# Kernel optimization log

Hardware: AMD Instinct MI355X
Metric: run time of the kernel (lower is better)

## Reference

```python
import jax, jax.numpy as jnp
import numpy as np

TEMPERATURE = 0.025

def _l2norm(x, eps=1e-12):
    # torch F.normalize(p=2, dim=-1): x / max(||x||, eps)
    n = jnp.sqrt(jnp.sum(x * x, axis=-1, keepdims=True))
    return x / jnp.maximum(n, eps)

def setup_inputs() -> dict:
    key = jax.random.key(0)
    ks = jax.random.split(key, 8)
    B, C, S = 512, 640, 14
    T = S * S  # 196
    H = T // 6  # 32
    sc1 = 1.0 / np.sqrt(T)
    sc2 = 1.0 / np.sqrt(H)
    return {
        "class_feat": jax.random.normal(ks[0], (B, C, S, S), jnp.float32),
        "query_feat": jax.random.normal(ks[1], (B, C, S, S), jnp.float32),
        "cw1": jax.random.normal(ks[2], (T, H), jnp.float32) * sc1,
        "cb1": jnp.zeros((H,), jnp.float32),
        "cw2": jax.random.normal(ks[3], (H, T), jnp.float32) * sc2,
        "cb2": jnp.zeros((T,), jnp.float32),
        "qw1": jax.random.normal(ks[4], (T, H), jnp.float32) * sc1,
        "qb1": jnp.zeros((H,), jnp.float32),
        "qw2": jax.random.normal(ks[5], (H, T), jnp.float32) * sc2,
        "qb2": jnp.zeros((T,), jnp.float32),
    }

def _apply_attention(feat, corr, w1, b1, w2, b2):
    # corr: [B, T, T]; kernel MLP on mean over dim=1 -> [B, T]
    B, C, S, _ = feat.shape
    m = corr.mean(axis=1)                              # [B, T]
    kernel = jax.nn.relu(m @ w1 + b1) @ w2 + b2        # [B, T]
    logits = jnp.einsum('btu,bu->bt', corr, kernel) / TEMPERATURE
    attn = jax.nn.softmax(logits, axis=1)              # softmax over tokens
    return feat * (1.0 + attn.reshape(B, 1, S, S))

def reference(class_feat, query_feat, cw1, cb1, cw2, cb2, qw1, qb1, qw2, qb2):
    B, C, S, _ = class_feat.shape
    T = S * S
    # tokens: [B, T, C], L2-normalized over channels
    ct = _l2norm(class_feat.reshape(B, C, T).transpose(0, 2, 1))
    qt = _l2norm(query_feat.reshape(B, C, T).transpose(0, 2, 1))
    corr = jnp.einsum('btc,buc->btu', ct, qt)          # [B, T, T]
    class_w = _apply_attention(class_feat, corr, cw1, cb1, cw2, cb2)
    query_w = _apply_attention(query_feat, corr.transpose(0, 2, 1), qw1, qb1, qw2, qb2)
    return (class_w, query_w)
```

## Files before the change

kernel.cpp:

```cpp
#include <hip/hip_runtime.h>

constexpr int kB = 512;
constexpr int kC = 640;
constexpr int kT = 196;
constexpr int kTP = 224;
constexpr int kH = 32;
constexpr int kKSTEP = 32;

typedef __bf16 bf16x8 __attribute__((ext_vector_type(8)));
typedef float  f32x16 __attribute__((ext_vector_type(16)));

__device__ __forceinline__ unsigned f2bfbits(float x) {
  unsigned u = __builtin_bit_cast(unsigned, x);
  return (u + 0x7FFFu + ((u >> 16) & 1u)) >> 16;
}
__device__ __forceinline__ float bf2f(unsigned short v) {
  return __builtin_bit_cast(float, (unsigned)v << 16);
}

__global__ __launch_bounds__(448) void corr_kernel(
    const float* __restrict__ cf, const float* __restrict__ qf,
    unsigned short* __restrict__ corr_out)
{
  __shared__ int Al[(kKSTEP/2) * kTP];
  __shared__ int Bl[(kKSTEP/2) * kTP];
  __shared__ float ssA[kTP], ssB[kTP], invA[kTP], invB[kTP];

  const int b    = blockIdx.x;
  const int tid  = threadIdx.x;
  const int wave = tid >> 6;
  const int lane = tid & 63;
  const int hf   = lane >> 5;
  const int l31  = lane & 31;

  const float4* Ap = (const float4*)(cf + (size_t)b * kC * kT);
  const float4* Bp = (const float4*)(qf + (size_t)b * kC * kT);

  const int t4 = tid % 56;
  const int kr = tid / 56;
  const bool realcol = (t4 < 49);

  if (tid < kTP) { ssA[tid] = 0.f; ssB[tid] = 0.f; }

  float4 sa = {0.f,0.f,0.f,0.f}, sb = {0.f,0.f,0.f,0.f};

  f32x16 acc[7];
#pragma unroll
  for (int c = 0; c < 7; ++c)
#pragma unroll
    for (int r = 0; r < 16; ++r) acc[c][r] = 0.f;

  const int mrow = 32 * wave + l31;

  for (int s = 0; s < kC / kKSTEP; ++s) {
    const int k0 = s * kKSTEP;
    __syncthreads();
#pragma unroll
    for (int i = 0; i < 2; ++i) {
      const int k2 = kr + 8 * i;
      float4 a0 = {0,0,0,0}, a1 = {0,0,0,0}, b0 = {0,0,0,0}, b1 = {0,0,0,0};
      if (realcol) {
        const size_t r0 = (size_t)(k0 + 2 * k2) * 49 + t4;
        a0 = Ap[r0]; a1 = Ap[r0 + 49];
        b0 = Bp[r0]; b1 = Bp[r0 + 49];
      }
      sa.x += a0.x*a0.x + a1.x*a1.x;  sa.y += a0.y*a0.y + a1.y*a1.y;
      sa.z += a0.z*a0.z + a1.z*a1.z;  sa.w += a0.w*a0.w + a1.w*a1.w;
      sb.x += b0.x*b0.x + b1.x*b1.x;  sb.y += b0.y*b0.y + b1.y*b1.y;
      sb.z += b0.z*b0.z + b1.z*b1.z;  sb.w += b0.w*b0.w + b1.w*b1.w;
      uint4 aw, bw;
      aw.x = f2bfbits(a0.x) | (f2bfbits(a1.x) << 16);
      aw.y = f2bfbits(a0.y) | (f2bfbits(a1.y) << 16);
      aw.z = f2bfbits(a0.z) | (f2bfbits(a1.z) << 16);
      aw.w = f2bfbits(a0.w) | (f2bfbits(a1.w) << 16);
      bw.x = f2bfbits(b0.x) | (f2bfbits(b1.x) << 16);
      bw.y = f2bfbits(b0.y) | (f2bfbits(b1.y) << 16);
      bw.z = f2bfbits(b0.z) | (f2bfbits(b1.z) << 16);
      bw.w = f2bfbits(b0.w) | (f2bfbits(b1.w) << 16);
      ((uint4*)Al)[k2 * 56 + t4] = aw;
      ((uint4*)Bl)[k2 * 56 + t4] = bw;
    }
    __syncthreads();
#pragma unroll
    for (int kk = 0; kk < 2; ++kk) {
      const int base = (kk * 8 + hf * 4) * kTP;
      int4 av;
      av.x = Al[base          + mrow];
      av.y = Al[base + kTP    + mrow];
      av.z = Al[base + 2*kTP  + mrow];
      av.w = Al[base + 3*kTP  + mrow];
      bf16x8 af = __builtin_bit_cast(bf16x8, av);
#pragma unroll
      for (int c = 0; c < 7; ++c) {
        const int nrow = 32 * c + l31;
        int4 bv;
        bv.x = Bl[base          + nrow];
        bv.y = Bl[base + kTP    + nrow];
        bv.z = Bl[base + 2*kTP  + nrow];
        bv.w = Bl[base + 3*kTP  + nrow];
        bf16x8 bfv = __builtin_bit_cast(bf16x8, bv);
        acc[c] = __builtin_amdgcn_mfma_f32_32x32x16_bf16(af, bfv, acc[c], 0, 0, 0);
      }
    }
  }

  if (realcol) {
    atomicAdd(&ssA[4*t4+0], sa.x); atomicAdd(&ssA[4*t4+1], sa.y);
    atomicAdd(&ssA[4*t4+2], sa.z); atomicAdd(&ssA[4*t4+3], sa.w);
    atomicAdd(&ssB[4*t4+0], sb.x); atomicAdd(&ssB[4*t4+1], sb.y);
    atomicAdd(&ssB[4*t4+2], sb.z); atomicAdd(&ssB[4*t4+3], sb.w);
  }
  __syncthreads();
  if (tid < kTP) {
    invA[tid] = 1.0f / fmaxf(sqrtf(ssA[tid]), 1e-12f);
    invB[tid] = 1.0f / fmaxf(sqrtf(ssB[tid]), 1e-12f);
  }
  __syncthreads();

  unsigned short* co = corr_out + (size_t)b * kT * kT;
#pragma unroll
  for (int c = 0; c < 7; ++c) {
    const int u = 32 * c + l31;
    if (u < kT) {
      const float ivu = invB[u];
#pragma unroll
      for (int r = 0; r < 16; ++r) {
        const int t = 32 * wave + (r & 3) + 8 * (r >> 2) + 4 * hf;
        if (t < kT) {
          co[t * kT + u] = (unsigned short)f2bfbits(acc[c][r] * invA[t] * ivu);
        }
      }
    }
  }
}

__device__ __forceinline__ void softmax196(float lgv, int tid, float* red, float* outp) {
  red[tid] = lgv;
  __syncthreads();
  for (int o = 128; o > 0; o >>= 1) {
    if (tid < o) red[tid] = fmaxf(red[tid], red[tid + o]);
    __syncthreads();
  }
  const float mx = red[0];
  __syncthreads();
  const float e = (tid < kT) ? __expf(lgv - mx) : 0.f;
  red[tid] = e;
  __syncthreads();
  for (int o = 128; o > 0; o >>= 1) {
    if (tid < o) red[tid] += red[tid + o];
    __syncthreads();
  }
  const float inv = 1.0f / red[0];
  if (tid < kT) outp[tid] = e * inv;
  __syncthreads();
}

__global__ __launch_bounds__(256) void attn_kernel(
    const unsigned short* __restrict__ corr,
    const float* __restrict__ w1c, const float* __restrict__ b1c,
    const float* __restrict__ w2c, const float* __restrict__ b2c,
    const float* __restrict__ w1q, const float* __restrict__ b1q,
    const float* __restrict__ w2q, const float* __restrict__ b2q,
    float* __restrict__ attnC, float* __restrict__ attnQ)
{
  __shared__ __align__(16) unsigned short cs[kT * kT];
  __shared__ float mC[kT], mQ[kT], hid[kH], kern[kT], red[256];

  const int b = blockIdx.x, tid = threadIdx.x;
  {
    const uint4* src = (const uint4*)(corr + (size_t)b * kT * kT);
    uint4* dst = (uint4*)cs;
    for (int i = tid; i < kT * kT / 8; i += 256) dst[i] = src[i];
  }
  __syncthreads();

  if (tid < kT) {
    float s = 0.f, s2 = 0.f;
    for (int t = 0; t < kT; ++t) s  += bf2f(cs[t * kT + tid]);
    for (int u = 0; u < kT; ++u) s2 += bf2f(cs[tid * kT + u]);
    mC[tid] = s  * (1.0f / kT);
    mQ[tid] = s2 * (1.0f / kT);
  }
  __syncthreads();

  if (tid < kH) {
    float s = b1c[tid];
    for (int u = 0; u < kT; ++u) s += mC[u] * w1c[u * kH + tid];
    hid[tid] = fmaxf(s, 0.f);
  }
  __syncthreads();
  if (tid < kT) {
    float s = b2c[tid];
    for (int h = 0; h < kH; ++h) s += hid[h] * w2c[h * kT + tid];
    kern[tid] = s;
  }
  __syncthreads();
  float lgv = -3.4e38f;
  if (tid < kT) {
    float s = 0.f;
    for (int u = 0; u < kT; ++u) s += bf2f(cs[tid * kT + u]) * kern[u];
    lgv = s * 40.0f;
  }
  softmax196(lgv, tid, red, attnC + (size_t)b * kT);

  if (tid < kH) {
    float s = b1q[tid];
    for (int u = 0; u < kT; ++u) s += mQ[u] * w1q[u * kH + tid];
    hid[tid] = fmaxf(s, 0.f);
  }
  __syncthreads();
  if (tid < kT) {
    float s = b2q[tid];
    for (int h = 0; h < kH; ++h) s += hid[h] * w2q[h * kT + tid];
    kern[tid] = s;
  }
  __syncthreads();
  lgv = -3.4e38f;
  if (tid < kT) {
    float s = 0.f;
    for (int t = 0; t < kT; ++t) s += bf2f(cs[t * kT + tid]) * kern[t];
    lgv = s * 40.0f;
  }
  softmax196(lgv, tid, red, attnQ + (size_t)b * kT);
}

__global__ __launch_bounds__(256) void scale_kernel(
    const float4* __restrict__ cf, const float4* __restrict__ qf,
    const float* __restrict__ attnC, const float* __restrict__ attnQ,
    float4* __restrict__ out)
{
  constexpr unsigned NC4 = (unsigned)kB * kC * 49u;
  const unsigned i = blockIdx.x * 256u + threadIdx.x;
  unsigned j;
  const float4* fp;
  const float* ap;
  if (i < NC4) { j = i;       fp = cf; ap = attnC; }
  else         { j = i - NC4; fp = qf; ap = attnQ; }
  const unsigned col = j % 49u;
  const unsigned bc  = j / 49u;
  const unsigned b   = bc / (unsigned)kC;
  const float4 f = fp[j];
  const float4 a = *(const float4*)(ap + (size_t)b * kT + col * 4u);
  float4 r;
  r.x = f.x * (1.f + a.x);
  r.y = f.y * (1.f + a.y);
  r.z = f.z * (1.f + a.z);
  r.w = f.w * (1.f + a.w);
  out[i] = r;
}

extern "C" void kernel_launch(void* const* d_in, const int* in_sizes, int n_in,
                              void* d_out, int out_size, void* d_ws, size_t ws_size,
                              hipStream_t stream) {
  const float* cf  = (const float*)d_in[0];
  const float* qf  = (const float*)d_in[1];
  const float* cw1 = (const float*)d_in[2];
  const float* cb1 = (const float*)d_in[3];
  const float* cw2 = (const float*)d_in[4];
  const float* cb2 = (const float*)d_in[5];
  const float* qw1 = (const float*)d_in[6];
  const float* qb1 = (const float*)d_in[7];
  const float* qw2 = (const float*)d_in[8];
  const float* qb2 = (const float*)d_in[9];
  float* out = (float*)d_out;

  char* ws = (char*)d_ws;
  unsigned short* corr = (unsigned short*)ws;
  float* attn_c = (float*)(ws + (size_t)kB * kT * kT * 2);
  float* attn_q = attn_c + (size_t)kB * kT;

  corr_kernel<<<kB, 448, 0, stream>>>(cf, qf, corr);
  attn_kernel<<<kB, 256, 0, stream>>>(corr, cw1, cb1, cw2, cb2,
                                      qw1, qb1, qw2, qb2, attn_c, attn_q);
  constexpr unsigned total4 = 2u * (unsigned)kB * kC * 49u;
  scale_kernel<<<total4 / 256u, 256, 0, stream>>>(
      (const float4*)cf, (const float4*)qf, attn_c, attn_q, (float4*)out);
}
```

Measured before the change: 963.7 us.

## Fuse correlation and attention kernels, computing MLP and logits from MFMA registers

Merges the correlation GEMM kernel with the attention kernel so the 196x196 correlation matrix stays in MFMA accumulator registers. Row and column means and both logit matvecs are computed there with shuffles and shared atomics, so the bf16 corr matrix is never written to or reread from global memory. The K loop is also double-buffered in LDS, with the next slice's global loads prefetched into registers so only one barrier is needed per step. This removes a kernel launch and the corr round trip, at the cost of more LDS and register pressure and an fp32 rather than bf16-rounded correlation.

```diff
diff --git a/kernel.cpp b/kernel.cpp
--- a/kernel.cpp
+++ b/kernel.cpp
@@ -6,6 +6,7 @@
 constexpr int kTP = 224;
 constexpr int kH = 32;
 constexpr int kKSTEP = 32;
+constexpr int kNS = kC / kKSTEP;
 
 typedef __bf16 bf16x8 __attribute__((ext_vector_type(8)));
 typedef float  f32x16 __attribute__((ext_vector_type(16)));
@@ -14,17 +15,23 @@
   unsigned u = __builtin_bit_cast(unsigned, x);
   return (u + 0x7FFFu + ((u >> 16) & 1u)) >> 16;
 }
-__device__ __forceinline__ float bf2f(unsigned short v) {
-  return __builtin_bit_cast(float, (unsigned)v << 16);
-}
-
-__global__ __launch_bounds__(448) void corr_kernel(
+
+__global__ __launch_bounds__(448) void fused_corr_attn(
     const float* __restrict__ cf, const float* __restrict__ qf,
-    unsigned short* __restrict__ corr_out)
+    const float* __restrict__ w1c, const float* __restrict__ b1c,
+    const float* __restrict__ w2c, const float* __restrict__ b2c,
+    const float* __restrict__ w1q, const float* __restrict__ b1q,
+    const float* __restrict__ w2q, const float* __restrict__ b2q,
+    float* __restrict__ attnC, float* __restrict__ attnQ)
 {
-  __shared__ int Al[(kKSTEP/2) * kTP];
-  __shared__ int Bl[(kKSTEP/2) * kTP];
+  __shared__ int Al[2][(kKSTEP/2) * kTP];
+  __shared__ int Bl[2][(kKSTEP/2) * kTP];
   __shared__ float ssA[kTP], ssB[kTP], invA[kTP], invB[kTP];
+  __shared__ float colsum[kTP], rowsum[kTP];
+  __shared__ float hidC[kH], hidQ[kH];
+  __shared__ float kernC[kTP], kernQ[kTP];
+  __shared__ float lgC[kTP], lgQ[kTP];
+  __shared__ float red[256];
 
   const int b    = blockIdx.x;
   const int tid  = threadIdx.x;
@@ -40,7 +47,12 @@
   const int kr = tid / 56;
   const bool realcol = (t4 < 49);
 
-  if (tid < kTP) { ssA[tid] = 0.f; ssB[tid] = 0.f; }
+  if (tid < kTP) {
+    ssA[tid] = 0.f; ssB[tid] = 0.f;
+    colsum[tid] = 0.f; lgQ[tid] = 0.f;
+  }
+  if (tid < kH)        hidC[tid] = 0.f;
+  else if (tid < 2*kH) hidQ[tid - kH] = 0.f;
 
   float4 sa = {0.f,0.f,0.f,0.f}, sb = {0.f,0.f,0.f,0.f};
 
@@ -52,18 +64,26 @@
 
   const int mrow = 32 * wave + l31;
 
-  for (int s = 0; s < kC / kKSTEP; ++s) {
-    const int k0 = s * kKSTEP;
-    __syncthreads();
+  float4 pa0[2], pa1[2], pb0[2], pb1[2];
+#pragma unroll
+  for (int i = 0; i < 2; ++i) {
+    pa0[i] = make_float4(0.f,0.f,0.f,0.f); pa1[i] = pa0[i];
+    pb0[i] = pa0[i];                        pb1[i] = pa0[i];
+    const int k2 = kr + 8 * i;
+    if (realcol) {
+      const size_t r0 = (size_t)(2 * k2) * 49 + t4;
+      pa0[i] = Ap[r0]; pa1[i] = Ap[r0 + 49];
+      pb0[i] = Bp[r0]; pb1[i] = Bp[r0 + 49];
+    }
+  }
+
+  for (int s = 0; s < kNS; ++s) {
+    uint4* Aw = (uint4*)Al[s & 1];
+    uint4* Bw = (uint4*)Bl[s & 1];
 #pragma unroll
     for (int i = 0; i < 2; ++i) {
       const int k2 = kr + 8 * i;
-      float4 a0 = {0,0,0,0}, a1 = {0,0,0,0}, b0 = {0,0,0,0}, b1 = {0,0,0,0};
-      if (realcol) {
-        const size_t r0 = (size_t)(k0 + 2 * k2) * 49 + t4;
-        a0 = Ap[r0]; a1 = Ap[r0 + 49];
-        b0 = Bp[r0]; b1 = Bp[r0 + 49];
-      }
+      const float4 a0 = pa0[i], a1 = pa1[i], b0 = pb0[i], b1 = pb1[i];
       sa.x += a0.x*a0.x + a1.x*a1.x;  sa.y += a0.y*a0.y + a1.y*a1.y;
       sa.z += a0.z*a0.z + a1.z*a1.z;  sa.w += a0.w*a0.w + a1.w*a1.w;
       sb.x += b0.x*b0.x + b1.x*b1.x;  sb.y += b0.y*b0.y + b1.y*b1.y;
@@ -77,27 +97,41 @@
       bw.y = f2bfbits(b0.y) | (f2bfbits(b1.y) << 16);
       bw.z = f2bfbits(b0.z) | (f2bfbits(b1.z) << 16);
       bw.w = f2bfbits(b0.w) | (f2bfbits(b1.w) << 16);
-      ((uint4*)Al)[k2 * 56 + t4] = aw;
-      ((uint4*)Bl)[k2 * 56 + t4] = bw;
-    }
-    __syncthreads();
+      Aw[k2 * 56 + t4] = aw;
+      Bw[k2 * 56 + t4] = bw;
+    }
+    if (s + 1 < kNS) {
+      const int k0n = (s + 1) * kKSTEP;
+#pragma unroll
+      for (int i = 0; i < 2; ++i) {
+        const int k2 = kr + 8 * i;
+        if (realcol) {
+          const size_t r0 = (size_t)(k0n + 2 * k2) * 49 + t4;
+          pa0[i] = Ap[r0]; pa1[i] = Ap[r0 + 49];
+          pb0[i] = Bp[r0]; pb1[i] = Bp[r0 + 49];
+        }
+      }
+    }
+    __syncthreads();
+    const int* Ar = Al[s & 1];
+    const int* Br = Bl[s & 1];
 #pragma unroll
     for (int kk = 0; kk < 2; ++kk) {
       const int base = (kk * 8 + hf * 4) * kTP;
       int4 av;
-      av.x = Al[base          + mrow];
-      av.y = Al[base + kTP    + mrow];
-      av.z = Al[base + 2*kTP  + mrow];
-      av.w = Al[base + 3*kTP  + mrow];
+      av.x = Ar[base          + mrow];
+      av.y = Ar[base + kTP    + mrow];
+      av.z = Ar[base + 2*kTP  + mrow];
+      av.w = Ar[base + 3*kTP  + mrow];
       bf16x8 af = __builtin_bit_cast(bf16x8, av);
 #pragma unroll
       for (int c = 0; c < 7; ++c) {
         const int nrow = 32 * c + l31;
         int4 bv;
-        bv.x = Bl[base          + nrow];
-        bv.y = Bl[base + kTP    + nrow];
-        bv.z = Bl[base + 2*kTP  + nrow];
-        bv.w = Bl[base + 3*kTP  + nrow];
+        bv.x = Br[base          + nrow];
+        bv.y = Br[base + kTP    + nrow];
+        bv.z = Br[base + 2*kTP  + nrow];
+        bv.w = Br[base + 3*kTP  + nrow];
         bf16x8 bfv = __builtin_bit_cast(bf16x8, bv);
         acc[c] = __builtin_amdgcn_mfma_f32_32x32x16_bf16(af, bfv, acc[c], 0, 0, 0);
       }
@@ -117,111 +151,141 @@
   }
   __syncthreads();
 
-  unsigned short* co = corr_out + (size_t)b * kT * kT;
+  float ia[16], ib[7];
+#pragma unroll
+  for (int r = 0; r < 16; ++r) ia[r] = invA[32*wave + 4*hf + (r&3) + 8*(r>>2)];
+#pragma unroll
+  for (int c = 0; c < 7; ++c) ib[c] = invB[32*c + l31];
+#pragma unroll
+  for (int c = 0; c < 7; ++c)
+#pragma unroll
+    for (int r = 0; r < 16; ++r) acc[c][r] *= ia[r] * ib[c];
+
 #pragma unroll
   for (int c = 0; c < 7; ++c) {
-    const int u = 32 * c + l31;
+    float s = 0.f;
+#pragma unroll
+    for (int r = 0; r < 16; ++r) s += acc[c][r];
+    s += __shfl_xor(s, 32);
+    if (hf == 0) atomicAdd(&colsum[32*c + l31], s);
+  }
+  {
+#pragma unroll
+    for (int r = 0; r < 16; ++r) {
+      float s = 0.f;
+#pragma unroll
+      for (int c = 0; c < 7; ++c) s += acc[c][r];
+#pragma unroll
+      for (int m = 1; m < 32; m <<= 1) s += __shfl_xor(s, m);
+      if (l31 == 0) rowsum[32*wave + 4*hf + (r&3) + 8*(r>>2)] = s;
+    }
+  }
+  __syncthreads();
+
+  {
+    const int half = tid / kTP;
+    const int h    = tid & 31;
+    const int grp  = (tid - half * kTP) >> 5;
+    const float* w1 = half ? w1q : w1c;
+    const float* ms = half ? rowsum : colsum;
+    float* hid      = half ? hidQ : hidC;
+    float s = 0.f;
+    const int u0 = grp * 28;
+    for (int u = u0; u < u0 + 28; ++u) s += ms[u] * w1[u * kH + h];
+    atomicAdd(&hid[h], s * (1.0f / (float)kT));
+  }
+  __syncthreads();
+  if (tid < kH)        hidC[tid]      = fmaxf(hidC[tid]      + b1c[tid],      0.f);
+  else if (tid < 2*kH) hidQ[tid - kH] = fmaxf(hidQ[tid - kH] + b1q[tid - kH], 0.f);
+  __syncthreads();
+
+  if (tid < kTP) {
+    const int u = tid;
+    float s = 0.f;
     if (u < kT) {
-      const float ivu = invB[u];
-#pragma unroll
-      for (int r = 0; r < 16; ++r) {
-        const int t = 32 * wave + (r & 3) + 8 * (r >> 2) + 4 * hf;
-        if (t < kT) {
-          co[t * kT + u] = (unsigned short)f2bfbits(acc[c][r] * invA[t] * ivu);
-        }
-      }
-    }
-  }
-}
-
-__device__ __forceinline__ void softmax196(float lgv, int tid, float* red, float* outp) {
-  red[tid] = lgv;
-  __syncthreads();
-  for (int o = 128; o > 0; o >>= 1) {
-    if (tid < o) red[tid] = fmaxf(red[tid], red[tid + o]);
-    __syncthreads();
-  }
-  const float mx = red[0];
-  __syncthreads();
-  const float e = (tid < kT) ? __expf(lgv - mx) : 0.f;
-  red[tid] = e;
-  __syncthreads();
-  for (int o = 128; o > 0; o >>= 1) {
-    if (tid < o) red[tid] += red[tid + o];
-    __syncthreads();
-  }
-  const float inv = 1.0f / red[0];
-  if (tid < kT) outp[tid] = e * inv;
-  __syncthreads();
-}
-
-__global__ __launch_bounds__(256) void attn_kernel(
-    const unsigned short* __restrict__ corr,
-    const float* __restrict__ w1c, const float* __restrict__ b1c,
-    const float* __restrict__ w2c, const float* __restrict__ b2c,
-    const float* __restrict__ w1q, const float* __restrict__ b1q,
-    const float* __restrict__ w2q, const float* __restrict__ b2q,
-    float* __restrict__ attnC, float* __restrict__ attnQ)
-{
-  __shared__ __align__(16) unsigned short cs[kT * kT];
-  __shared__ float mC[kT], mQ[kT], hid[kH], kern[kT], red[256];
-
-  const int b = blockIdx.x, tid = threadIdx.x;
-  {
-    const uint4* src = (const uint4*)(corr + (size_t)b * kT * kT);
-    uint4* dst = (uint4*)cs;
-    for (int i = tid; i < kT * kT / 8; i += 256) dst[i] = src[i];
-  }
-  __syncthreads();
-
-  if (tid < kT) {
-    float s = 0.f, s2 = 0.f;
-    for (int t = 0; t < kT; ++t) s  += bf2f(cs[t * kT + tid]);
-    for (int u = 0; u < kT; ++u) s2 += bf2f(cs[tid * kT + u]);
-    mC[tid] = s  * (1.0f / kT);
-    mQ[tid] = s2 * (1.0f / kT);
-  }
-  __syncthreads();
-
-  if (tid < kH) {
-    float s = b1c[tid];
-    for (int u = 0; u < kT; ++u) s += mC[u] * w1c[u * kH + tid];
-    hid[tid] = fmaxf(s, 0.f);
-  }
-  __syncthreads();
-  if (tid < kT) {
-    float s = b2c[tid];
-    for (int h = 0; h < kH; ++h) s += hid[h] * w2c[h * kT + tid];
-    kern[tid] = s;
-  }
-  __syncthreads();
-  float lgv = -3.4e38f;
-  if (tid < kT) {
+      s = b2c[u];
+      for (int h = 0; h < kH; ++h) s += hidC[h] * w2c[h * kT + u];
+    }
+    kernC[u] = s;
+  } else {
+    const int u = tid - kTP;
     float s = 0.f;
-    for (int u = 0; u < kT; ++u) s += bf2f(cs[tid * kT + u]) * kern[u];
-    lgv = s * 40.0f;
-  }
-  softmax196(lgv, tid, red, attnC + (size_t)b * kT);
-
-  if (tid < kH) {
-    float s = b1q[tid];
-    for (int u = 0; u < kT; ++u) s += mQ[u] * w1q[u * kH + tid];
-    hid[tid] = fmaxf(s, 0.f);
-  }
-  __syncthreads();
-  if (tid < kT) {
-    float s = b2q[tid];
-    for (int h = 0; h < kH; ++h) s += hid[h] * w2q[h * kT + tid];
-    kern[tid] = s;
-  }
-  __syncthreads();
-  lgv = -3.4e38f;
-  if (tid < kT) {
-    float s = 0.f;
-    for (int t = 0; t < kT; ++t) s += bf2f(cs[t * kT + tid]) * kern[t];
-    lgv = s * 40.0f;
-  }
-  softmax196(lgv, tid, red, attnQ + (size_t)b * kT);
+    if (u < kT) {
+      s = b2q[u];
+      for (int h = 0; h < kH; ++h) s += hidQ[h] * w2q[h * kT + u];
+    }
+    kernQ[u] = s;
+  }
+  __syncthreads();
+
+  {
+    float kc[7];
+#pragma unroll
+    for (int c = 0; c < 7; ++c) kc[c] = kernC[32*c + l31];
+#pragma unroll
+    for (int r = 0; r < 16; ++r) {
+      float s = 0.f;
+#pragma unroll
+      for (int c = 0; c < 7; ++c) s += acc[c][r] * kc[c];
+#pragma unroll
+      for (int m = 1; m < 32; m <<= 1) s += __shfl_xor(s, m);
+      if (l31 == 0) lgC[32*wave + 4*hf + (r&3) + 8*(r>>2)] = s;
+    }
+    float kq[16];
+#pragma unroll
+    for (int r = 0; r < 16; ++r) kq[r] = kernQ[32*wave + 4*hf + (r&3) + 8*(r>>2)];
+#pragma unroll
+    for (int c = 0; c < 7; ++c) {
+      float s = 0.f;
+#pragma unroll
+      for (int r = 0; r < 16; ++r) s += acc[c][r] * kq[r];
+      s += __shfl_xor(s, 32);
+      if (hf == 0) atomicAdd(&lgQ[32*c + l31], s);
+    }
+  }
+  __syncthreads();
+
+  {
+    float lv = (tid < kT) ? lgC[tid] * 40.f : -3.4e38f;
+    if (tid < 256) red[tid] = lv;
+    __syncthreads();
+    for (int o = 128; o > 0; o >>= 1) {
+      if (tid < o) red[tid] = fmaxf(red[tid], red[tid + o]);
+      __syncthreads();
+    }
+    const float mx = red[0];
+    __syncthreads();
+    const float e = (tid < kT) ? __expf(lv - mx) : 0.f;
+    if (tid < 256) red[tid] = e;
+    __syncthreads();
+    for (int o = 128; o > 0; o >>= 1) {
+      if (tid < o) red[tid] += red[tid + o];
+      __syncthreads();
+    }
+    const float inv = 1.0f / red[0];
+    if (tid < kT) attnC[(size_t)b * kT + tid] = e * inv;
+    __syncthreads();
+  }
+  {
+    float lv = (tid < kT) ? lgQ[tid] * 40.f : -3.4e38f;
+    if (tid < 256) red[tid] = lv;
+    __syncthreads();
+    for (int o = 128; o > 0; o >>= 1) {
+      if (tid < o) red[tid] = fmaxf(red[tid], red[tid + o]);
+      __syncthreads();
+    }
+    const float mx = red[0];
+    __syncthreads();
+    const float e = (tid < kT) ? __expf(lv - mx) : 0.f;
+    if (tid < 256) red[tid] = e;
+    __syncthreads();
+    for (int o = 128; o > 0; o >>= 1) {
+      if (tid < o) red[tid] += red[tid + o];
+      __syncthreads();
+    }
+    const float inv = 1.0f / red[0];
+    if (tid < kT) attnQ[(size_t)b * kT + tid] = e * inv;
+  }
 }
 
 __global__ __launch_bounds__(256) void scale_kernel(
@@ -264,14 +328,11 @@
   const float* qb2 = (const float*)d_in[9];
   float* out = (float*)d_out;
 
-  char* ws = (char*)d_ws;
-  unsigned short* corr = (unsigned short*)ws;
-  float* attn_c = (float*)(ws + (size_t)kB * kT * kT * 2);
+  float* attn_c = (float*)d_ws;
   float* attn_q = attn_c + (size_t)kB * kT;
 
-  corr_kernel<<<kB, 448, 0, stream>>>(cf, qf, corr);
-  attn_kernel<<<kB, 256, 0, stream>>>(corr, cw1, cb1, cw2, cb2,
-                                      qw1, qb1, qw2, qb2, attn_c, attn_q);
+  fused_corr_attn<<<kB, 448, 0, stream>>>(cf, qf, cw1, cb1, cw2, cb2,
+                                          qw1, qb1, qw2, qb2, attn_c, attn_q);
   constexpr unsigned total4 = 2u * (unsigned)kB * kC * 49u;
   scale_kernel<<<total4 / 256u, 256, 0, stream>>>(
       (const float4*)cf, (const float4*)qf, attn_c, attn_q, (float4*)out);
```

After: 931.7 us. -3.3%, faster.
